# Performance work log

Hardware: AMD Instinct MI355X
Metric: run time of the kernel (lower is better)

## Reference

```python
import jax, jax.numpy as jnp
import numpy as np

# Multi-scale feature pyramid (H, W) per level: strides 8/16/32/64 on a ~512px image
SHAPES = ((64, 64), (32, 32), (16, 16), (8, 8))
N_HEADS, N_LEVELS, N_POINTS = 8, 4, 4
D_MODEL = 256
HEAD_DIM = D_MODEL // N_HEADS


def setup_inputs() -> dict:
    key = jax.random.key(0)
    ks = jax.random.split(key, 11)
    B, C = 4, D_MODEL
    Lv = sum(h * w for h, w in SHAPES)  # 5440
    Lq = Lv  # encoder self-attention: queries are the flattened features
    scale = 0.02
    return {
        "query": jax.random.normal(ks[0], (B, Lq, C), jnp.float32),
        "reference_points": jax.random.uniform(ks[1], (B, Lq, N_LEVELS, 2), jnp.float32),
        "value": jax.random.normal(ks[2], (B, Lv, C), jnp.float32),
        "W_off": jax.random.normal(ks[3], (C, N_HEADS * N_LEVELS * N_POINTS * 2), jnp.float32) * scale,
        "b_off": jax.random.normal(ks[4], (N_HEADS * N_LEVELS * N_POINTS * 2,), jnp.float32) * 0.5,
        "W_attn": jax.random.normal(ks[5], (C, N_HEADS * N_LEVELS * N_POINTS), jnp.float32) * scale,
        "b_attn": jax.random.normal(ks[6], (N_HEADS * N_LEVELS * N_POINTS,), jnp.float32) * scale,
        "W_val": jax.random.normal(ks[7], (C, C), jnp.float32) * scale,
        "b_val": jax.random.normal(ks[8], (C,), jnp.float32) * scale,
        "W_out": jax.random.normal(ks[9], (C, C), jnp.float32) * scale,
        "b_out": jax.random.normal(ks[10], (C,), jnp.float32) * scale,
    }


def _bilinear_sample(val, grid, H, W):
    """Replicates F.grid_sample(mode='bilinear', padding_mode='zeros', align_corners=False).

    val:  [N, C, H, W]
    grid: [N, Lq, P, 2] in [-1, 1] (x, y order)
    returns: [N, C, Lq, P]
    """
    N, C = val.shape[0], val.shape[1]
    # unnormalize (align_corners=False)
    x = (grid[..., 0] + 1.0) * 0.5 * W - 0.5  # [N, Lq, P]
    y = (grid[..., 1] + 1.0) * 0.5 * H - 0.5
    x0 = jnp.floor(x)
    y0 = jnp.floor(y)
    wx = x - x0  # fractional parts
    wy = y - y0
    flat = val.reshape(N, C, H * W)

    def gather(xi, yi):
        valid = (xi >= 0) & (xi < W) & (yi >= 0) & (yi < H)
        xc = jnp.clip(xi, 0, W - 1).astype(jnp.int32)
        yc = jnp.clip(yi, 0, H - 1).astype(jnp.int32)
        idx = yc * W + xc  # [N, Lq, P]
        g = jax.vmap(lambda v, i: v[:, i])(flat, idx)  # [N, C, Lq, P]
        return g * valid[:, None, :, :].astype(val.dtype)

    out = (gather(x0, y0) * ((1 - wx) * (1 - wy))[:, None]
           + gather(x0 + 1, y0) * (wx * (1 - wy))[:, None]
           + gather(x0, y0 + 1) * ((1 - wx) * wy)[:, None]
           + gather(x0 + 1, y0 + 1) * (wx * wy)[:, None])
    return out


def _ms_deform_attn(query, reference_points, value, W_off, b_off, W_attn, b_attn,
                    W_val, b_val, W_out, b_out):
    B, Lq, C = query.shape
    val = value @ W_val + b_val  # [B, Lv, C]
    val = val.reshape(B, -1, N_HEADS, HEAD_DIM)

    offsets = (query @ W_off + b_off).reshape(B, Lq, N_HEADS, N_LEVELS, N_POINTS, 2)
    weights = jax.nn.softmax(
        (query @ W_attn + b_attn).reshape(B, Lq, N_HEADS, N_LEVELS * N_POINTS), axis=-1
    ).reshape(B, Lq, N_HEADS, N_LEVELS, N_POINTS)

    # offset normalizer: (W, H) per level
    offset_norm = jnp.array([[w, h] for h, w in SHAPES], jnp.float32)
    # ref_dim == 2 branch
    locs = reference_points[:, :, None, :, None, :] + offsets / offset_norm[None, None, None, :, None, :]
    grids = 2.0 * locs - 1.0  # [B, Lq, nh, nl, np, 2]

    acc = jnp.zeros((B * N_HEADS, HEAD_DIM, Lq), query.dtype)
    start = 0
    for lid, (H, W) in enumerate(SHAPES):
        # [B, HW, nh, hd] -> [B*nh, hd, H, W]
        v = val[:, start:start + H * W].transpose(0, 2, 3, 1).reshape(B * N_HEADS, HEAD_DIM, H, W)
        g = grids[:, :, :, lid].transpose(0, 2, 1, 3, 4).reshape(B * N_HEADS, Lq, N_POINTS, 2)
        s = _bilinear_sample(v, g, H, W)  # [B*nh, hd, Lq, np]
        w = weights[:, :, :, lid].transpose(0, 2, 1, 3).reshape(B * N_HEADS, 1, Lq, N_POINTS)
        acc = acc + (s * w).sum(-1)
        start += H * W

    out = acc.reshape(B, D_MODEL, Lq).transpose(0, 2, 1)  # [B, Lq, C]
    return out @ W_out + b_out


def reference(query, reference_points, value, W_off, b_off, W_attn, b_attn,
              W_val, b_val, W_out, b_out):
    return _ms_deform_attn(query, reference_points, value, W_off, b_off,
                           W_attn, b_attn, W_val, b_val, W_out, b_out)
```

## Files before the change

### kernel.cpp

```cpp
#include <hip/hip_runtime.h>


typedef __attribute__((ext_vector_type(8))) _Float16 half8;
typedef __attribute__((ext_vector_type(4))) float f32x4;

typedef __attribute__((address_space(3))) unsigned int lds_uint;
typedef const __attribute__((address_space(1))) unsigned int g_uint;

__device__ __forceinline__ void load_lds16(const _Float16* g, _Float16* l) {
    __builtin_amdgcn_global_load_lds((g_uint*)g, (lds_uint*)l, 16, 0, 0);
}

__device__ __forceinline__ half8 splat8(_Float16 v) {
    half8 r = {v, v, v, v, v, v, v, v};
    return r;
}

#define M_TOTAL 21760

__global__ __launch_bounds__(256) void gemm12_cvt(
    const float* __restrict__ value, const float* __restrict__ query,
    const float* __restrict__ W_val, const float* __restrict__ W_off,
    const float* __restrict__ W_attn,
    const float* __restrict__ b_val, const float* __restrict__ b_off,
    const float* __restrict__ b_attn,
    _Float16* __restrict__ valh, _Float16* __restrict__ offh)
{
    __shared__ _Float16 As[128 * 34];
    __shared__ _Float16 Bs[128 * 34];

    const bool g1 = blockIdx.x < 340;
    const int id = g1 ? blockIdx.x : blockIdx.x - 340;
    const int mt = g1 ? (id >> 1) : (id / 3);
    const int nt = g1 ? (id & 1) : (id % 3);
    const int NN = g1 ? 256 : 384;
    const float* A = g1 ? value : query;
    _Float16* C = g1 ? valh : offh;
    const int bm = mt * 128;
    const int bn = nt * 128;

    const float* W;
    int sW, nb;
    if (g1)            { W = W_val;  sW = 256; nb = bn; }
    else if (nt < 2)   { W = W_off;  sW = 256; nb = bn; }
    else               { W = W_attn; sW = 128; nb = 0;  }

    const int tid = threadIdx.x;
    const int wave = tid >> 6, lane = tid & 63;
    const int wm = (wave & 1) * 64, wn = (wave >> 1) * 64;
    const int ml = lane & 15, kq = (lane >> 4) * 8;

    const int ar = tid >> 1, akb = (tid & 1) * 16;
    const int bn_l = tid & 127, bkg = (tid >> 7) * 16;

    const f32x4 zero4 = {0.f, 0.f, 0.f, 0.f};
    f32x4 acc[4][4];
#pragma unroll
    for (int i = 0; i < 4; ++i)
#pragma unroll
        for (int j = 0; j < 4; ++j) acc[i][j] = zero4;

    for (int kt = 0; kt < 8; ++kt) {
        const int k0 = kt * 32;
        const float* as = A + (size_t)(bm + ar) * 256 + k0 + akb;
        const float4 a0 = *(const float4*)(as + 0);
        const float4 a1 = *(const float4*)(as + 4);
        const float4 a2 = *(const float4*)(as + 8);
        const float4 a3 = *(const float4*)(as + 12);
        float bv[16];
#pragma unroll
        for (int j = 0; j < 16; ++j)
            bv[j] = W[(size_t)(k0 + bkg + j) * sW + nb + bn_l];

        const half8 ha0 = {(_Float16)a0.x, (_Float16)a0.y, (_Float16)a0.z, (_Float16)a0.w,
                           (_Float16)a1.x, (_Float16)a1.y, (_Float16)a1.z, (_Float16)a1.w};
        const half8 ha1 = {(_Float16)a2.x, (_Float16)a2.y, (_Float16)a2.z, (_Float16)a2.w,
                           (_Float16)a3.x, (_Float16)a3.y, (_Float16)a3.z, (_Float16)a3.w};
        const half8 hb0 = {(_Float16)bv[0], (_Float16)bv[1], (_Float16)bv[2], (_Float16)bv[3],
                           (_Float16)bv[4], (_Float16)bv[5], (_Float16)bv[6], (_Float16)bv[7]};
        const half8 hb1 = {(_Float16)bv[8], (_Float16)bv[9], (_Float16)bv[10], (_Float16)bv[11],
                           (_Float16)bv[12], (_Float16)bv[13], (_Float16)bv[14], (_Float16)bv[15]};

        __syncthreads();
        *(half8*)(As + ar * 34 + akb) = ha0;
        *(half8*)(As + ar * 34 + akb + 8) = ha1;
        *(half8*)(Bs + bn_l * 34 + bkg) = hb0;
        *(half8*)(Bs + bn_l * 34 + bkg + 8) = hb1;
        __syncthreads();

        half8 af[4], bf[4];
#pragma unroll
        for (int i = 0; i < 4; ++i)
            af[i] = *(const half8*)(As + (wm + i * 16 + ml) * 34 + kq);
#pragma unroll
        for (int j = 0; j < 4; ++j)
            bf[j] = *(const half8*)(Bs + (wn + j * 16 + ml) * 34 + kq);
#pragma unroll
        for (int i = 0; i < 4; ++i)
#pragma unroll
            for (int j = 0; j < 4; ++j)
                acc[i][j] = __builtin_amdgcn_mfma_f32_16x16x32_f16(af[i], bf[j], acc[i][j], 0, 0, 0);
    }

    const int r0 = (lane >> 4) * 4;
#pragma unroll
    for (int j = 0; j < 4; ++j) {
        const int col = bn + wn + j * 16 + ml;
        const float bj = g1 ? b_val[col] : (col < 256 ? b_off[col] : b_attn[col - 256]);
#pragma unroll
        for (int i = 0; i < 4; ++i) {
            const size_t rbase = (size_t)(bm + wm + i * 16 + r0) * NN + col;
#pragma unroll
            for (int r = 0; r < 4; ++r)
                C[rbase + (size_t)r * NN] = (_Float16)(acc[i][j][r] + bj);
        }
    }
}

__device__ __forceinline__ void gemm_core(
    const _Float16* __restrict__ A, const _Float16* __restrict__ Bt,
    const float* __restrict__ bias, float* __restrict__ Cv,
    int NN, int mt, int nt)
{
    __shared__ _Float16 Ah[128 * 32];
    __shared__ _Float16 Bh[64 * 32];

    const int tid = threadIdx.x;
    const int bm = mt * 128;
    const int bn = nt * 64;
    const int wave = tid >> 6, lane = tid & 63;
    const int wm = (wave & 1) * 64, wn = (wave >> 1) * 32;
    const int ml = lane & 15, kq = (lane >> 4) * 8;
    const int lr = lane >> 2;
    const int lk = (lane & 3) * 8;

    const f32x4 zero4 = {0.f, 0.f, 0.f, 0.f};
    f32x4 acc[4][2];
#pragma unroll
    for (int i = 0; i < 4; ++i)
#pragma unroll
        for (int j = 0; j < 2; ++j) acc[i][j] = zero4;

    for (int kt = 0; kt < 8; ++kt) {
        const int k0 = kt * 32;
        __syncthreads();
#pragma unroll
        for (int t = 0; t < 2; ++t) {
            const int row = wave * 32 + t * 16;
            load_lds16(A + (size_t)(bm + row + lr) * 256 + k0 + lk,
                       Ah + (size_t)row * 32);
        }
        {
            const int row = wave * 16;
            load_lds16(Bt + (size_t)(bn + row + lr) * 256 + k0 + lk,
                       Bh + (size_t)row * 32);
        }
        __syncthreads();

        half8 af[4], bf[2];
#pragma unroll
        for (int i = 0; i < 4; ++i)
            af[i] = *(const half8*)(Ah + (wm + i * 16 + ml) * 32 + kq);
#pragma unroll
        for (int j = 0; j < 2; ++j)
            bf[j] = *(const half8*)(Bh + (wn + j * 16 + ml) * 32 + kq);
#pragma unroll
        for (int i = 0; i < 4; ++i)
#pragma unroll
            for (int j = 0; j < 2; ++j)
                acc[i][j] = __builtin_amdgcn_mfma_f32_16x16x32_f16(af[i], bf[j], acc[i][j], 0, 0, 0);
    }

    const int r0 = (lane >> 4) * 4;
#pragma unroll
    for (int j = 0; j < 2; ++j) {
        const int col = bn + wn + j * 16 + ml;
        const float bj = bias[col];
#pragma unroll
        for (int i = 0; i < 4; ++i) {
            const size_t rbase = (size_t)(bm + wm + i * 16 + r0) * NN + col;
#pragma unroll
            for (int r = 0; r < 4; ++r)
                Cv[rbase + (size_t)r * NN] = acc[i][j][r] + bj;
        }
    }
}

__global__ __launch_bounds__(256) void gemm_single(
    const _Float16* __restrict__ A, const _Float16* __restrict__ Bt,
    const float* __restrict__ bias, float* __restrict__ Cv)
{
    const int id = blockIdx.x;
    gemm_core(A, Bt, bias, Cv, 256, id >> 2, id & 3);
}

__global__ __launch_bounds__(256, 4) void sample_f16(
    const _Float16* __restrict__ valh,
    const float* __restrict__ refp,
    const _Float16* __restrict__ offh,
    const float* __restrict__ W_out,
    _Float16* __restrict__ wto,
    _Float16* __restrict__ acc_out)
{
    if (blockIdx.x < 256)
        wto[blockIdx.x * 256 + threadIdx.x] =
            (_Float16)W_out[threadIdx.x * 256 + blockIdx.x];

    const int wave = threadIdx.x >> 6, lane = threadIdx.x & 63;
    const int q2 = lane >> 5, sl = lane & 31;
    const int bq = blockIdx.x * 8 + wave * 2 + q2;
    const int b = bq / 5440;
    const int h = sl >> 2;
    const int d8 = (sl & 3) * 8;

    const _Float16* off_row = offh + (size_t)bq * 384 + h * 32;
    const _Float16* att_row = offh + (size_t)bq * 384 + 256 + h * 16;
    const float* rp = refp + (size_t)bq * 8;

    const half8 ofr0 = *(const half8*)(off_row);
    const half8 ofr1 = *(const half8*)(off_row + 8);
    const half8 ofr2 = *(const half8*)(off_row + 16);
    const half8 ofr3 = *(const half8*)(off_row + 24);
    float lg[16];
    {
        const half8 t0 = *(const half8*)(att_row);
        const half8 t1 = *(const half8*)(att_row + 8);
#pragma unroll
        for (int j = 0; j < 8; ++j) { lg[j] = (float)t0[j]; lg[8 + j] = (float)t1[j]; }
    }
    float mx = -1e30f;
#pragma unroll
    for (int i = 0; i < 16; ++i) mx = fmaxf(mx, lg[i]);
    float s = 0.f;
#pragma unroll
    for (int i = 0; i < 16; ++i) { lg[i] = __expf(lg[i] - mx); s += lg[i]; }
    const float inv = 1.f / s;

    const float4 rp01 = *(const float4*)rp;
    const float4 rp23 = *(const float4*)(rp + 4);
    const float rxs[4] = {rp01.x, rp01.z, rp23.x, rp23.z};
    const float rys[4] = {rp01.y, rp01.w, rp23.y, rp23.w};

    const int Ws_[4] = {64, 32, 16, 8};
    const int starts_[4] = {0, 4096, 5120, 5376};

    half8 acc = splat8((_Float16)0.f);
#pragma unroll
    for (int l = 0; l < 4; ++l) {
        const int W = Ws_[l];
        const float fW = (float)W;
        const _Float16* vbase = valh + ((size_t)(b * 5440 + starts_[l])) * 256 + h * 32 + d8;
        const float rx = rxs[l], ry = rys[l];

        int idx_[16];
        _Float16 w_[16];
#pragma unroll
        for (int p = 0; p < 4; ++p) {
            const int pi = l * 4 + p;
            const float aw = lg[pi] * inv;
            float ox, oy;
            {
                const half8 src = (pi < 8) ? ((pi < 4) ? ofr0 : ofr1)
                                           : ((pi < 12) ? ofr2 : ofr3);
                const int e = (pi & 3) * 2;
                ox = (float)src[e];
                oy = (float)src[e + 1];
            }
            const float x = fmaf(rx, fW, ox) - 0.5f;
            const float y = fmaf(ry, fW, oy) - 0.5f;
            const float x0f = floorf(x), y0f = floorf(y);
            const int x0 = (int)x0f, y0 = (int)y0f;
            const float wx = x - x0f, wy = y - y0f;
            const bool okx0 = ((unsigned)x0 < (unsigned)W);
            const bool okx1 = ((unsigned)(x0 + 1) < (unsigned)W);
            const bool oky0 = ((unsigned)y0 < (unsigned)W);
            const bool oky1 = ((unsigned)(y0 + 1) < (unsigned)W);
            const int xc0 = min(max(x0, 0), W - 1);
            const int xc1 = min(max(x0 + 1, 0), W - 1);
            const int yc0 = min(max(y0, 0), W - 1);
            const int yc1 = min(max(y0 + 1, 0), W - 1);
            w_[p * 4 + 0] = (_Float16)((okx0 & oky0) ? (1.f - wx) * (1.f - wy) * aw : 0.f);
            w_[p * 4 + 1] = (_Float16)((okx1 & oky0) ? wx * (1.f - wy) * aw : 0.f);
            w_[p * 4 + 2] = (_Float16)((okx0 & oky1) ? (1.f - wx) * wy * aw : 0.f);
            w_[p * 4 + 3] = (_Float16)((okx1 & oky1) ? wx * wy * aw : 0.f);
            idx_[p * 4 + 0] = (yc0 * W + xc0) * 256;
            idx_[p * 4 + 1] = (yc0 * W + xc1) * 256;
            idx_[p * 4 + 2] = (yc1 * W + xc0) * 256;
            idx_[p * 4 + 3] = (yc1 * W + xc1) * 256;
        }

        __builtin_amdgcn_sched_barrier(0);
        half8 c_[16];
#pragma unroll
        for (int i = 0; i < 16; ++i)
            c_[i] = *(const half8*)(vbase + idx_[i]);
        __builtin_amdgcn_sched_barrier(0);
#pragma unroll
        for (int i = 0; i < 16; ++i)
            acc += c_[i] * splat8(w_[i]);
    }

    *(half8*)(acc_out + (size_t)bq * 256 + h * 32 + d8) = acc;
}

extern "C" void kernel_launch(void* const* d_in, const int* in_sizes, int n_in,
                              void* d_out, int out_size, void* d_ws, size_t ws_size,
                              hipStream_t stream) {
    const float* query  = (const float*)d_in[0];
    const float* refp   = (const float*)d_in[1];
    const float* value  = (const float*)d_in[2];
    const float* W_off  = (const float*)d_in[3];
    const float* b_off  = (const float*)d_in[4];
    const float* W_attn = (const float*)d_in[5];
    const float* b_attn = (const float*)d_in[6];
    const float* W_val  = (const float*)d_in[7];
    const float* b_val  = (const float*)d_in[8];
    const float* W_out  = (const float*)d_in[9];
    const float* b_out  = (const float*)d_in[10];
    float* out = (float*)d_out;

    const size_t M = M_TOTAL;

    _Float16* valh  = (_Float16*)d_ws;
    _Float16* offh  = valh + M * 256;
    _Float16* acc16 = offh + M * 384;
    _Float16* wto   = acc16 + M * 256;

    dim3 blk(256);
    gemm12_cvt<<<dim3(850), blk, 0, stream>>>(
        value, query, W_val, W_off, W_attn, b_val, b_off, b_attn, valh, offh);
    sample_f16<<<dim3(M / 8), blk, 0, stream>>>(valh, refp, offh, W_out, wto, acc16);
    gemm_single<<<dim3(680), blk, 0, stream>>>(acc16, wto, b_out, out);
}
```

Baseline: 175.1 us.

## Preload full weight tile to LDS and stream A fragments directly from global

The fused projection GEMM now converts the whole 256x128 weight slice to fp16 and stores it once in LDS in an MFMA-friendly layout, with a single barrier up front. The A operand no longer goes through LDS. Each lane loads its own MFMA fragment straight from global memory, and the next k-step is register-prefetched while the current one computes. This removes the two per-iteration barriers and the LDS round trip for A. In exchange, LDS use grows to 64KB, which may lower occupancy, and the two wave columns load the same A rows redundantly from global.

```diff
diff --git a/kernel.cpp b/kernel.cpp
--- a/kernel.cpp
+++ b/kernel.cpp
@@ -26,8 +26,7 @@
     const float* __restrict__ b_attn,
     _Float16* __restrict__ valh, _Float16* __restrict__ offh)
 {
-    __shared__ _Float16 As[128 * 34];
-    __shared__ _Float16 Bs[128 * 34];
+    __shared__ _Float16 Bs[32 * 128 * 8];
 
     const bool g1 = blockIdx.x < 340;
     const int id = g1 ? blockIdx.x : blockIdx.x - 340;
@@ -50,8 +49,21 @@
     const int wm = (wave & 1) * 64, wn = (wave >> 1) * 64;
     const int ml = lane & 15, kq = (lane >> 4) * 8;
 
-    const int ar = tid >> 1, akb = (tid & 1) * 16;
-    const int bn_l = tid & 127, bkg = (tid >> 7) * 16;
+    {
+        const int n_l = tid & 127;
+        const int kh = tid >> 7;
+#pragma unroll
+        for (int ko = 0; ko < 128; ko += 8) {
+            const int k = kh * 128 + ko;
+            half8 h;
+#pragma unroll
+            for (int e = 0; e < 8; ++e)
+                h[e] = (_Float16)W[(size_t)(k + e) * sW + nb + n_l];
+            const int kt = k >> 5, g = (k >> 3) & 3;
+            *(half8*)(Bs + ((kt * 4 + g) * 128 + n_l) * 8) = h;
+        }
+    }
+    __syncthreads();
 
     const f32x4 zero4 = {0.f, 0.f, 0.f, 0.f};
     f32x4 acc[4][4];
@@ -60,41 +72,38 @@
 #pragma unroll
         for (int j = 0; j < 4; ++j) acc[i][j] = zero4;
 
+    const float* ap = A + (size_t)(bm + wm + ml) * 256 + kq;
+    const _Float16* bsp = Bs + ((size_t)(lane >> 4) * 128 + wn + ml) * 8;
+
+    float4 pa[4][2];
+#pragma unroll
+    for (int i = 0; i < 4; ++i) {
+        const float* p = ap + (size_t)i * 16 * 256;
+        pa[i][0] = *(const float4*)(p);
+        pa[i][1] = *(const float4*)(p + 4);
+    }
+
     for (int kt = 0; kt < 8; ++kt) {
-        const int k0 = kt * 32;
-        const float* as = A + (size_t)(bm + ar) * 256 + k0 + akb;
-        const float4 a0 = *(const float4*)(as + 0);
-        const float4 a1 = *(const float4*)(as + 4);
-        const float4 a2 = *(const float4*)(as + 8);
-        const float4 a3 = *(const float4*)(as + 12);
-        float bv[16];
-#pragma unroll
-        for (int j = 0; j < 16; ++j)
-            bv[j] = W[(size_t)(k0 + bkg + j) * sW + nb + bn_l];
-
-        const half8 ha0 = {(_Float16)a0.x, (_Float16)a0.y, (_Float16)a0.z, (_Float16)a0.w,
-                           (_Float16)a1.x, (_Float16)a1.y, (_Float16)a1.z, (_Float16)a1.w};
-        const half8 ha1 = {(_Float16)a2.x, (_Float16)a2.y, (_Float16)a2.z, (_Float16)a2.w,
-                           (_Float16)a3.x, (_Float16)a3.y, (_Float16)a3.z, (_Float16)a3.w};
-        const half8 hb0 = {(_Float16)bv[0], (_Float16)bv[1], (_Float16)bv[2], (_Float16)bv[3],
-                           (_Float16)bv[4], (_Float16)bv[5], (_Float16)bv[6], (_Float16)bv[7]};
-        const half8 hb1 = {(_Float16)bv[8], (_Float16)bv[9], (_Float16)bv[10], (_Float16)bv[11],
-                           (_Float16)bv[12], (_Float16)bv[13], (_Float16)bv[14], (_Float16)bv[15]};
-
-        __syncthreads();
-        *(half8*)(As + ar * 34 + akb) = ha0;
-        *(half8*)(As + ar * 34 + akb + 8) = ha1;
-        *(half8*)(Bs + bn_l * 34 + bkg) = hb0;
-        *(half8*)(Bs + bn_l * 34 + bkg + 8) = hb1;
-        __syncthreads();
-
-        half8 af[4], bf[4];
-#pragma unroll
-        for (int i = 0; i < 4; ++i)
-            af[i] = *(const half8*)(As + (wm + i * 16 + ml) * 34 + kq);
+        half8 af[4];
+#pragma unroll
+        for (int i = 0; i < 4; ++i) {
+            const float4 a0 = pa[i][0];
+            const float4 a1 = pa[i][1];
+            af[i] = (half8){(_Float16)a0.x, (_Float16)a0.y, (_Float16)a0.z, (_Float16)a0.w,
+                            (_Float16)a1.x, (_Float16)a1.y, (_Float16)a1.z, (_Float16)a1.w};
+        }
+        if (kt < 7) {
+#pragma unroll
+            for (int i = 0; i < 4; ++i) {
+                const float* p = ap + (size_t)i * 16 * 256 + (kt + 1) * 32;
+                pa[i][0] = *(const float4*)(p);
+                pa[i][1] = *(const float4*)(p + 4);
+            }
+        }
+        half8 bf[4];
 #pragma unroll
         for (int j = 0; j < 4; ++j)
-            bf[j] = *(const half8*)(Bs + (wn + j * 16 + ml) * 34 + kq);
+            bf[j] = *(const half8*)(bsp + ((size_t)kt * 4 * 128 + j * 16) * 8);
 #pragma unroll
         for (int i = 0; i < 4; ++i)
 #pragma unroll
```

Result: slower. 190.9 us (+9.0%).

## Double-buffer LDS and prefetch next K tile in fused projection GEMM

Applied to the files above, without the earlier changes.

The fp32-to-fp16 projection GEMM now uses two LDS buffers and register-prefetches the next K tile's global data while the current tile is being consumed, cutting one barrier per iteration. The LDS layout also changes from a padded row-major tile (stride 34) to a k-group-major layout of 8-element chunks, so fragment reads are contiguous 16-byte loads. The intent is to hide global load latency behind the MFMA work and avoid LDS bank conflicts. In exchange it doubles LDS use and raises register pressure from the prefetch registers.

```diff
diff --git a/kernel.cpp b/kernel.cpp
--- a/kernel.cpp
+++ b/kernel.cpp
@@ -26,8 +26,8 @@
     const float* __restrict__ b_attn,
     _Float16* __restrict__ valh, _Float16* __restrict__ offh)
 {
-    __shared__ _Float16 As[128 * 34];
-    __shared__ _Float16 Bs[128 * 34];
+    __shared__ _Float16 Af[2][4 * 128 * 8];
+    __shared__ _Float16 Bf[2][4 * 128 * 8];
 
     const bool g1 = blockIdx.x < 340;
     const int id = g1 ? blockIdx.x : blockIdx.x - 340;
@@ -48,10 +48,45 @@
     const int tid = threadIdx.x;
     const int wave = tid >> 6, lane = tid & 63;
     const int wm = (wave & 1) * 64, wn = (wave >> 1) * 64;
-    const int ml = lane & 15, kq = (lane >> 4) * 8;
-
-    const int ar = tid >> 1, akb = (tid & 1) * 16;
-    const int bn_l = tid & 127, bkg = (tid >> 7) * 16;
+    const int ml = lane & 15;
+    const int gq = lane >> 4;
+
+    const int sr = tid & 127;
+    const int sg = tid >> 7;
+
+    const float* aS = A + (size_t)(bm + sr) * 256 + sg * 16;
+    const float* wS = W + (size_t)(sg * 16) * sW + nb + sr;
+
+    float4 pa0, pa1, pa2, pa3;
+    float pb[16];
+
+    auto LOAD = [&](int kt) {
+        const float* p = aS + kt * 32;
+        pa0 = *(const float4*)(p + 0);
+        pa1 = *(const float4*)(p + 4);
+        pa2 = *(const float4*)(p + 8);
+        pa3 = *(const float4*)(p + 12);
+        const float* q = wS + (size_t)kt * 32 * sW;
+#pragma unroll
+        for (int e = 0; e < 16; ++e) pb[e] = q[(size_t)e * sW];
+    };
+
+    auto WRITE = [&](int buf) {
+        const half8 ha0 = {(_Float16)pa0.x, (_Float16)pa0.y, (_Float16)pa0.z, (_Float16)pa0.w,
+                           (_Float16)pa1.x, (_Float16)pa1.y, (_Float16)pa1.z, (_Float16)pa1.w};
+        const half8 ha1 = {(_Float16)pa2.x, (_Float16)pa2.y, (_Float16)pa2.z, (_Float16)pa2.w,
+                           (_Float16)pa3.x, (_Float16)pa3.y, (_Float16)pa3.z, (_Float16)pa3.w};
+        const half8 hb0 = {(_Float16)pb[0], (_Float16)pb[1], (_Float16)pb[2], (_Float16)pb[3],
+                           (_Float16)pb[4], (_Float16)pb[5], (_Float16)pb[6], (_Float16)pb[7]};
+        const half8 hb1 = {(_Float16)pb[8], (_Float16)pb[9], (_Float16)pb[10], (_Float16)pb[11],
+                           (_Float16)pb[12], (_Float16)pb[13], (_Float16)pb[14], (_Float16)pb[15]};
+        _Float16* ab = &Af[buf][0];
+        _Float16* bb = &Bf[buf][0];
+        *(half8*)(ab + (((sg * 2) * 128 + sr) << 3)) = ha0;
+        *(half8*)(ab + (((sg * 2 + 1) * 128 + sr) << 3)) = ha1;
+        *(half8*)(bb + (((sg * 2) * 128 + sr) << 3)) = hb0;
+        *(half8*)(bb + (((sg * 2 + 1) * 128 + sr) << 3)) = hb1;
+    };
 
     const f32x4 zero4 = {0.f, 0.f, 0.f, 0.f};
     f32x4 acc[4][4];
@@ -60,46 +95,28 @@
 #pragma unroll
         for (int j = 0; j < 4; ++j) acc[i][j] = zero4;
 
+    LOAD(0);
+    int cur = 0;
     for (int kt = 0; kt < 8; ++kt) {
-        const int k0 = kt * 32;
-        const float* as = A + (size_t)(bm + ar) * 256 + k0 + akb;
-        const float4 a0 = *(const float4*)(as + 0);
-        const float4 a1 = *(const float4*)(as + 4);
-        const float4 a2 = *(const float4*)(as + 8);
-        const float4 a3 = *(const float4*)(as + 12);
-        float bv[16];
-#pragma unroll
-        for (int j = 0; j < 16; ++j)
-            bv[j] = W[(size_t)(k0 + bkg + j) * sW + nb + bn_l];
-
-        const half8 ha0 = {(_Float16)a0.x, (_Float16)a0.y, (_Float16)a0.z, (_Float16)a0.w,
-                           (_Float16)a1.x, (_Float16)a1.y, (_Float16)a1.z, (_Float16)a1.w};
-        const half8 ha1 = {(_Float16)a2.x, (_Float16)a2.y, (_Float16)a2.z, (_Float16)a2.w,
-                           (_Float16)a3.x, (_Float16)a3.y, (_Float16)a3.z, (_Float16)a3.w};
-        const half8 hb0 = {(_Float16)bv[0], (_Float16)bv[1], (_Float16)bv[2], (_Float16)bv[3],
-                           (_Float16)bv[4], (_Float16)bv[5], (_Float16)bv[6], (_Float16)bv[7]};
-        const half8 hb1 = {(_Float16)bv[8], (_Float16)bv[9], (_Float16)bv[10], (_Float16)bv[11],
-                           (_Float16)bv[12], (_Float16)bv[13], (_Float16)bv[14], (_Float16)bv[15]};
-
+        WRITE(cur);
+        if (kt < 7) LOAD(kt + 1);
         __syncthreads();
-        *(half8*)(As + ar * 34 + akb) = ha0;
-        *(half8*)(As + ar * 34 + akb + 8) = ha1;
-        *(half8*)(Bs + bn_l * 34 + bkg) = hb0;
-        *(half8*)(Bs + bn_l * 34 + bkg + 8) = hb1;
-        __syncthreads();
 
         half8 af[4], bf[4];
+        const _Float16* ab = &Af[cur][0] + ((size_t)gq * 128 << 3);
+        const _Float16* bb = &Bf[cur][0] + ((size_t)gq * 128 << 3);
 #pragma unroll
         for (int i = 0; i < 4; ++i)
-            af[i] = *(const half8*)(As + (wm + i * 16 + ml) * 34 + kq);
+            af[i] = *(const half8*)(ab + ((wm + i * 16 + ml) << 3));
 #pragma unroll
         for (int j = 0; j < 4; ++j)
-            bf[j] = *(const half8*)(Bs + (wn + j * 16 + ml) * 34 + kq);
+            bf[j] = *(const half8*)(bb + ((wn + j * 16 + ml) << 3));
 #pragma unroll
         for (int i = 0; i < 4; ++i)
 #pragma unroll
             for (int j = 0; j < 4; ++j)
                 acc[i][j] = __builtin_amdgcn_mfma_f32_16x16x32_f16(af[i], bf[j], acc[i][j], 0, 0, 0);
+        cur ^= 1;
     }
 
     const int r0 = (lane >> 4) * 4;
```

Result: no change. 172.5 us (-1.5%).
